# Kernel optimization log

Hardware: AMD Instinct MI355X
Metric: run time of the kernel (lower is better)

The kernel has to match this reference:

```python
import jax, jax.numpy as jnp
import numpy as np

L_PAIRS = 2
K_NEG = 64
TEMP = 0.1
EPS = 1e-8  # torch F.cosine_similarity default eps


def _cos(a, b):
    # cosine similarity along last axis, torch-style eps clamping of norms
    na = jnp.maximum(jnp.linalg.norm(a, axis=-1), EPS)
    nb = jnp.maximum(jnp.linalg.norm(b, axis=-1), EPS)
    return jnp.sum(a * b, axis=-1) / (na * nb)


def setup_inputs() -> dict:
    D, N, d = 64, 4096, 512
    key = jax.random.key(0)
    k0, k1, k2, k3 = jax.random.split(key, 4)
    return {
        "I_embeddings": jax.random.normal(k0, (D, N, d), dtype=jnp.float32),
        "g0": jax.random.normal(k1, (d,), dtype=jnp.float32),
        "g1": jax.random.normal(k2, (d,), dtype=jnp.float32),
        "g2": jax.random.normal(k3, (d,), dtype=jnp.float32),
    }


def reference(I_embeddings, g0, g1, g2):
    D, N, d = I_embeddings.shape
    T = TEMP

    # per-embedding full sum: [D, d]
    sums = jnp.sum(I_embeddings, axis=1)

    # hard-negative sums: drop the top-K rows by L2 norm per embedding
    norms = jnp.linalg.norm(I_embeddings, axis=2)              # [D, N]
    _, topk_idx = jax.lax.top_k(norms, K_NEG)                  # [D, K]
    keep = jnp.ones((D, N), dtype=bool)
    keep = keep.at[jnp.arange(D)[:, None], topk_idx].set(False)
    sums_neg = jnp.sum(I_embeddings * keep[:, :, None], axis=1)  # [D, d]

    samples = jnp.concatenate([sums, sums_neg], axis=0)        # [2D, d]

    # positive pairs (i, i+L)
    P = D - L_PAIRS
    i_idx = jnp.arange(P)
    j_idx = i_idx + L_PAIRS

    # candidates per pair: arange(2D) with i and j removed (i < j)
    base = jnp.arange(2 * D - 2)                               # [2D-2]
    cand = base[None, :] + (base[None, :] >= i_idx[:, None]).astype(base.dtype)
    cand = cand + (cand >= j_idx[:, None]).astype(cand.dtype)  # [P, 2D-2]

    # random choice of K_NEG negatives per pair (deterministic key)
    key = jax.random.key(42)
    keys = jax.random.split(key, P)
    perm = jax.vmap(lambda k: jax.random.permutation(k, 2 * D - 2))(keys)[:, :K_NEG]
    sel = jnp.take_along_axis(cand, perm, axis=1)              # [P, K]
    negs = samples[sel]                                        # [P, K, d]

    pos_ij = _cos(g1, jax.lax.stop_gradient(g2)) / T           # scalar
    pos_ji = _cos(g2, jax.lax.stop_gradient(g1)) / T           # scalar

    s_i = sums[i_idx]                                          # [P, d]
    s_j = sums[j_idx]
    sim_i = _cos(s_i[:, None, :], negs) / T                    # [P, K]
    sim_j = _cos(s_j[:, None, :], negs) / T

    # -log( exp(pos) / (exp(pos) + sum exp(sim)) ) = logaddexp(pos, lse(sim)) - pos
    loss_i = jnp.logaddexp(pos_ij, jax.nn.logsumexp(sim_i, axis=1)) - pos_ij  # [P]
    loss_j = jnp.logaddexp(pos_ji, jax.nn.logsumexp(sim_j, axis=1)) - pos_ji

    return jnp.sum(loss_i + loss_j)
```

## Files before the change

### kernel.cpp

```cpp
#include <hip/hip_runtime.h>
#include <stdint.h>

#define D_EMB   64
#define N_ROWS  4096
#define DIM     512
#define KNEG    64
#define P_PAIRS 62
#define BPE     16
#define RPB     (N_ROWS / BPE)
#define NCHUNK  (D_EMB * BPE)
#define EPSN    1e-8f
#define INV_T   10.0f
#define NEGINF  (-1e30f)

typedef float f32x4 __attribute__((ext_vector_type(4)));

__device__ __forceinline__ uint32_t rotl32(uint32_t v, uint32_t r) {
  return (v << r) | (v >> (32u - r));
}

__device__ __forceinline__ void threefry(uint32_t k0, uint32_t k1,
                                         uint32_t c0, uint32_t c1,
                                         uint32_t& o0, uint32_t& o1) {
  uint32_t ks0 = k0, ks1 = k1, ks2 = k0 ^ k1 ^ 0x1BD11BDAu;
  uint32_t x0 = c0 + ks0, x1 = c1 + ks1;
#define RG(a,b,c,d) \
  x0 += x1; x1 = rotl32(x1,a); x1 ^= x0; \
  x0 += x1; x1 = rotl32(x1,b); x1 ^= x0; \
  x0 += x1; x1 = rotl32(x1,c); x1 ^= x0; \
  x0 += x1; x1 = rotl32(x1,d); x1 ^= x0;
  RG(13,15,26,6)   x0 += ks1; x1 += ks2 + 1u;
  RG(17,29,16,24)  x0 += ks2; x1 += ks0 + 2u;
  RG(13,15,26,6)   x0 += ks0; x1 += ks1 + 3u;
  RG(17,29,16,24)  x0 += ks1; x1 += ks2 + 4u;
  RG(13,15,26,6)   x0 += ks2; x1 += ks0 + 5u;
#undef RG
  o0 = x0; o1 = x1;
}

__global__ __launch_bounds__(256, 4) void k_pass1(const float* __restrict__ I,
                                                  float* __restrict__ partial,
                                                  float* __restrict__ norms) {
  const int e = blockIdx.x >> 4, b = blockIdx.x & 15;
  const int t = threadIdx.x, lane = t & 63, w = t >> 6;
  const f32x4* base4 = reinterpret_cast<const f32x4*>(I) + (size_t)e * N_ROWS * (DIM / 4);
  const int nbase = b * RPB;
  const int wrow = w * (RPB / 4);
  __shared__ float lds[4 * DIM];
  __shared__ float nlds[RPB];
  float acc[8] = {0.f,0.f,0.f,0.f,0.f,0.f,0.f,0.f};

#define NTL(p) __builtin_nontemporal_load(p)
  for (int i = 0; i < 8; ++i) {
    const int lr = wrow + i * 8;
    const int idx = (nbase + lr) * (DIM / 4) + lane;
    f32x4 A0 = NTL(base4 + idx + 0*128), B0 = NTL(base4 + idx + 0*128 + 64);
    f32x4 A1 = NTL(base4 + idx + 1*128), B1 = NTL(base4 + idx + 1*128 + 64);
    f32x4 A2 = NTL(base4 + idx + 2*128), B2 = NTL(base4 + idx + 2*128 + 64);
    f32x4 A3 = NTL(base4 + idx + 3*128), B3 = NTL(base4 + idx + 3*128 + 64);
    f32x4 A4 = NTL(base4 + idx + 4*128), B4 = NTL(base4 + idx + 4*128 + 64);
    f32x4 A5 = NTL(base4 + idx + 5*128), B5 = NTL(base4 + idx + 5*128 + 64);
    f32x4 A6 = NTL(base4 + idx + 6*128), B6 = NTL(base4 + idx + 6*128 + 64);
    f32x4 A7 = NTL(base4 + idx + 7*128), B7 = NTL(base4 + idx + 7*128 + 64);
#undef NTL

    acc[0] += A0.x + A1.x + A2.x + A3.x + A4.x + A5.x + A6.x + A7.x;
    acc[1] += A0.y + A1.y + A2.y + A3.y + A4.y + A5.y + A6.y + A7.y;
    acc[2] += A0.z + A1.z + A2.z + A3.z + A4.z + A5.z + A6.z + A7.z;
    acc[3] += A0.w + A1.w + A2.w + A3.w + A4.w + A5.w + A6.w + A7.w;
    acc[4] += B0.x + B1.x + B2.x + B3.x + B4.x + B5.x + B6.x + B7.x;
    acc[5] += B0.y + B1.y + B2.y + B3.y + B4.y + B5.y + B6.y + B7.y;
    acc[6] += B0.z + B1.z + B2.z + B3.z + B4.z + B5.z + B6.z + B7.z;
    acc[7] += B0.w + B1.w + B2.w + B3.w + B4.w + B5.w + B6.w + B7.w;

#define SQ(r) (A##r.x*A##r.x + A##r.y*A##r.y + A##r.z*A##r.z + A##r.w*A##r.w \
             + B##r.x*B##r.x + B##r.y*B##r.y + B##r.z*B##r.z + B##r.w*B##r.w)
    float s0 = SQ(0), s1 = SQ(1), s2 = SQ(2), s3 = SQ(3);
    float s4 = SQ(4), s5 = SQ(5), s6 = SQ(6), s7 = SQ(7);
#undef SQ
#pragma unroll
    for (int off = 32; off; off >>= 1) {
      s0 += __shfl_xor(s0, off); s1 += __shfl_xor(s1, off);
      s2 += __shfl_xor(s2, off); s3 += __shfl_xor(s3, off);
      s4 += __shfl_xor(s4, off); s5 += __shfl_xor(s5, off);
      s6 += __shfl_xor(s6, off); s7 += __shfl_xor(s7, off);
    }
    if (lane == 0) {
      nlds[lr]     = sqrtf(s0); nlds[lr + 1] = sqrtf(s1);
      nlds[lr + 2] = sqrtf(s2); nlds[lr + 3] = sqrtf(s3);
      nlds[lr + 4] = sqrtf(s4); nlds[lr + 5] = sqrtf(s5);
      nlds[lr + 6] = sqrtf(s6); nlds[lr + 7] = sqrtf(s7);
    }
  }

  const int p0 = 4 * lane;
#pragma unroll
  for (int q = 0; q < 4; ++q) {
    lds[w * DIM + p0 + q]       = acc[q];
    lds[w * DIM + 256 + p0 + q] = acc[4 + q];
  }
  __syncthreads();
  float s0 = lds[t] + lds[DIM + t] + lds[2*DIM + t] + lds[3*DIM + t];
  float s1 = lds[256 + t] + lds[DIM + 256 + t] + lds[2*DIM + 256 + t] + lds[3*DIM + 256 + t];
  float* po = partial + (size_t)blockIdx.x * DIM;
  po[t] = s0;
  po[256 + t] = s1;
  norms[e * N_ROWS + nbase + t] = nlds[t];
}

#define CE(i, j) \
  { bool sw = (v##i < v##j) || (v##i == v##j && d##i > d##j);          \
    float tv = sw ? v##j : v##i; float uv = sw ? v##i : v##j;          \
    int   td = sw ? d##j : d##i; int   ud = sw ? d##i : d##j;          \
    v##i = tv; v##j = uv; d##i = td; d##j = ud; }

__global__ __launch_bounds__(512) void k_embed(const float* __restrict__ I,
                                               const float* __restrict__ partial,
                                               const float* __restrict__ norms,
                                               const float* __restrict__ g1,
                                               const float* __restrict__ g2,
                                               float* __restrict__ samples,
                                               float* __restrict__ snorm,
                                               float* __restrict__ posp,
                                               int* __restrict__ cnt2) {
  const int e = blockIdx.x;
  const int t = threadIdx.x, lane = t & 63, w = t >> 6;
  __shared__ float rA[8], rB[8], rC[8];

  if (e == D_EMB) {
    if (t == 0) cnt2[0] = 0;
    float x = g1[t], y = g2[t];
    float d = x * y, sa = x * x, sb = y * y;
#pragma unroll
    for (int off = 32; off; off >>= 1) {
      d  += __shfl_xor(d, off);
      sa += __shfl_xor(sa, off);
      sb += __shfl_xor(sb, off);
    }
    if (lane == 0) { rA[w] = d; rB[w] = sa; rC[w] = sb; }
    __syncthreads();
    if (t == 0) {
      float dt = 0.f, s1 = 0.f, s2 = 0.f;
      for (int q = 0; q < 8; ++q) { dt += rA[q]; s1 += rB[q]; s2 += rC[q]; }
      posp[0] = dt / (fmaxf(sqrtf(s1), EPSN) * fmaxf(sqrtf(s2), EPSN)) * INV_T;
    }
    return;
  }

  __shared__ float cval[8 * KNEG];
  __shared__ int   cidx[8 * KNEG];
  __shared__ int   topidx[KNEG];

  float v0 = norms[e*N_ROWS + 0*512 + t], v1 = norms[e*N_ROWS + 1*512 + t];
  float v2 = norms[e*N_ROWS + 2*512 + t], v3 = norms[e*N_ROWS + 3*512 + t];
  float v4 = norms[e*N_ROWS + 4*512 + t], v5 = norms[e*N_ROWS + 5*512 + t];
  float v6 = norms[e*N_ROWS + 6*512 + t], v7 = norms[e*N_ROWS + 7*512 + t];
  int d0 = 0*512+t, d1 = 1*512+t, d2 = 2*512+t, d3 = 3*512+t;
  int d4 = 4*512+t, d5 = 5*512+t, d6 = 6*512+t, d7 = 7*512+t;
  CE(0,1) CE(2,3) CE(4,5) CE(6,7)
  CE(0,2) CE(1,3) CE(4,6) CE(5,7)
  CE(1,2) CE(5,6)
  CE(0,4) CE(1,5) CE(2,6) CE(3,7)
  CE(2,4) CE(3,5)
  CE(1,2) CE(3,4) CE(5,6)

  for (int k = 0; k < KNEG; ++k) {
    float bv = v0; int bi = d0;
#pragma unroll
    for (int off = 32; off; off >>= 1) {
      float ov = __shfl_xor(bv, off);
      int   oi = __shfl_xor(bi, off);
      if (ov > bv || (ov == bv && oi < bi)) { bv = ov; bi = oi; }
    }
    if (lane == 0) { cval[w * KNEG + k] = bv; cidx[w * KNEG + k] = bi; }
    if (v0 == bv && d0 == bi) {
      v0=v1; d0=d1; v1=v2; d1=d2; v2=v3; d2=d3; v3=v4; d3=d4;
      v4=v5; d4=d5; v5=v6; d5=d6; v6=v7; d6=d7; v7=NEGINF; d7=0x7fffffff;
    }
  }
  __syncthreads();

  if (w == 0) {
    int p = 0;
    float hv = (lane < 8) ? cval[lane * KNEG] : NEGINF;
    int   hi = (lane < 8) ? cidx[lane * KNEG] : 0x7fffffff;
    for (int k = 0; k < KNEG; ++k) {
      float bv = hv; int bi = hi;
#pragma unroll
      for (int off = 4; off; off >>= 1) {
        float ov = __shfl_xor(bv, off, 8);
        int   oi = __shfl_xor(bi, off, 8);
        if (ov > bv || (ov == bv && oi < bi)) { bv = ov; bi = oi; }
      }
      if (lane == 0) topidx[k] = bi;
      if (lane < 8 && hv == bv && hi == bi) {
        ++p;
        hv = (p < KNEG) ? cval[lane * KNEG + p] : NEGINF;
        hi = (p < KNEG) ? cidx[lane * KNEG + p] : 0x7fffffff;
      }
    }
  }
  __syncthreads();

  float s = 0.f;
  for (int b2 = 0; b2 < BPE; ++b2)
    s += partial[(size_t)(e * BPE + b2) * DIM + t];

  const float* base = I + (size_t)e * N_ROWS * DIM;
  float a = 0.f;
#pragma unroll 4
  for (int k = 0; k < KNEG; ++k)
    a += base[(size_t)topidx[k] * DIM + t];
  float sn = s - a;

  float q1 = s * s, q2 = sn * sn;
#pragma unroll
  for (int off = 32; off; off >>= 1) {
    q1 += __shfl_xor(q1, off);
    q2 += __shfl_xor(q2, off);
  }
  if (lane == 0) { rA[w] = q1; rB[w] = q2; }
  __syncthreads();
  if (t == 0) {
    float n1 = 0.f, n2 = 0.f;
    for (int q = 0; q < 8; ++q) { n1 += rA[q]; n2 += rB[q]; }
    snorm[e]         = fmaxf(sqrtf(n1), EPSN);
    snorm[D_EMB + e] = fmaxf(sqrtf(n2), EPSN);
  }
  samples[(size_t)e * DIM + t]           = s;
  samples[(size_t)(D_EMB + e) * DIM + t] = sn;
}

__global__ __launch_bounds__(256) void k_p3p4(const float* __restrict__ samples,
                                              const float* __restrict__ snorm,
                                              const float* __restrict__ posp,
                                              float* __restrict__ pairloss,
                                              int* __restrict__ cnt2,
                                              float* __restrict__ out) {
  const int p = blockIdx.x;
  const int t = threadIdx.x, lane = t & 63, w = t >> 6;
  __shared__ uint32_t bits[126];
  __shared__ uint32_t sk[2];
  __shared__ int      sel[KNEG];
  __shared__ float    simi[KNEG], simj[KNEG];
  __shared__ int      flag;

  if (t == 0) {
    uint32_t kh, kl, a, b;
    threefry(0u, 42u, 0u, (uint32_t)p, kh, kl);
    threefry(kh, kl, 0u, 1u, a, b);
    sk[0] = a; sk[1] = b;
  }
  __syncthreads();
  if (t < 126) {
    uint32_t a, b;
    threefry(sk[0], sk[1], 0u, (uint32_t)t, a, b);
    bits[t] = a ^ b;
  }
  __syncthreads();
  if (t < 126) {
    const uint32_t myb = bits[t];
    int rank = 0;
    for (int j = 0; j < 126; ++j) {
      const uint32_t bj = bits[j];
      rank += ((bj < myb) || (bj == myb && j < t)) ? 1 : 0;
    }
    if (rank < KNEG) {
      int vv = t + (t >= p ? 1 : 0);
      vv += (vv >= p + 2 ? 1 : 0);
      sel[rank] = vv;
    }
  }
  __syncthreads();

  const float4* S = reinterpret_cast<const float4*>(samples);
  const float4 siA = S[p * 128 + lane],       siB = S[p * 128 + 64 + lane];
  const float4 sjA = S[(p + 2) * 128 + lane], sjB = S[(p + 2) * 128 + 64 + lane];
  const float ni = snorm[p], nj = snorm[p + 2];
  for (int k = w; k < KNEG; k += 4) {
    const int r = sel[k];
    const float4 vA = S[r * 128 + lane], vB = S[r * 128 + 64 + lane];
    float di = siA.x*vA.x + siA.y*vA.y + siA.z*vA.z + siA.w*vA.w
             + siB.x*vB.x + siB.y*vB.y + siB.z*vB.z + siB.w*vB.w;
    float dj = sjA.x*vA.x + sjA.y*vA.y + sjA.z*vA.z + sjA.w*vA.w
             + sjB.x*vB.x + sjB.y*vB.y + sjB.z*vB.z + sjB.w*vB.w;
#pragma unroll
    for (int off = 32; off; off >>= 1) {
      di += __shfl_xor(di, off);
      dj += __shfl_xor(dj, off);
    }
    if (lane == 0) {
      const float nr = snorm[r];
      simi[k] = di / (ni * nr) * INV_T;
      simj[k] = dj / (nj * nr) * INV_T;
    }
  }
  __syncthreads();
  if (t < KNEG) {
    const float xi = simi[t], xj = simj[t];
    float mi = xi, mj = xj;
#pragma unroll
    for (int off = 32; off; off >>= 1) {
      mi = fmaxf(mi, __shfl_xor(mi, off));
      mj = fmaxf(mj, __shfl_xor(mj, off));
    }
    float ei = expf(xi - mi), ej = expf(xj - mj);
#pragma unroll
    for (int off = 32; off; off >>= 1) {
      ei += __shfl_xor(ei, off);
      ej += __shfl_xor(ej, off);
    }
    if (t == 0) {
      const float pos = posp[0];
      const float lsei = mi + logf(ei), lsej = mj + logf(ej);
      const float li = fmaxf(pos, lsei) + log1pf(expf(-fabsf(pos - lsei))) - pos;
      const float lj = fmaxf(pos, lsej) + log1pf(expf(-fabsf(pos - lsej))) - pos;
      pairloss[p] = li + lj;
    }
  }
  __syncthreads();

  if (t == 0) {
    int old = __hip_atomic_fetch_add(cnt2, 1, __ATOMIC_ACQ_REL,
                                     __HIP_MEMORY_SCOPE_AGENT);
    flag = (old == P_PAIRS - 1) ? 1 : 0;
  }
  __syncthreads();
  const int trig = flag;
  __syncthreads();
  if (!trig) return;
  __builtin_amdgcn_fence(__ATOMIC_ACQUIRE, "agent");
  if (t < 64) {
    float vv = (t < P_PAIRS) ? pairloss[t] : 0.f;
#pragma unroll
    for (int off = 32; off; off >>= 1) vv += __shfl_xor(vv, off);
    if (t == 0) out[0] = vv;
  }
}

extern "C" void kernel_launch(void* const* d_in, const int* in_sizes, int n_in,
                              void* d_out, int out_size, void* d_ws, size_t ws_size,
                              hipStream_t stream) {
  const float* I  = (const float*)d_in[0];
  const float* g1 = (const float*)d_in[2];
  const float* g2 = (const float*)d_in[3];
  float* out = (float*)d_out;

  float* ws = (float*)d_ws;
  float* norms    = ws;
  float* partial  = ws + 262144;
  float* samples  = partial + 524288;
  float* snorm    = samples + 65536;
  float* posp     = snorm + 128;
  float* pairloss = posp + 4;
  int*   cnt2     = (int*)(pairloss + 64);

  k_pass1<<<NCHUNK,    256, 0, stream>>>(I, partial, norms);
  k_embed<<<D_EMB + 1, 512, 0, stream>>>(I, partial, norms, g1, g2,
                                         samples, snorm, posp, cnt2);
  k_p3p4 <<<P_PAIRS,   256, 0, stream>>>(samples, snorm, posp, pairloss,
                                         cnt2, out);
}
```

Measured before the change: 177.2 us.

## Fuse pass1 and per-embedding top-k via last-block atomic counter

Merges the streaming sum/norm kernel with the per-embedding top-k and sample-building kernel. Each block bumps a per-embedding atomic counter, and the last of the 16 blocks for an embedding runs the top-k, the hard-negative subtraction and the sample norms, using 256 threads. This removes one kernel launch and the gap between kernels, and lets the tail work overlap with streaming for other embeddings. The top-k now keeps a 16-value per-lane buffer with rescans in place of a sorting network, and a memset is added to reset the counters. The risk is that the last-arriving blocks carry serial top-k work, while the tail runs at half the thread count and shares LDS with the streaming blocks.

```diff
diff --git a/kernel.cpp b/kernel.cpp
--- a/kernel.cpp
+++ b/kernel.cpp
@@ -38,16 +38,48 @@
   o0 = x0; o1 = x1;
 }
 
-__global__ __launch_bounds__(256, 4) void k_pass1(const float* __restrict__ I,
-                                                  float* __restrict__ partial,
-                                                  float* __restrict__ norms) {
+__global__ __launch_bounds__(256, 4) void k_p1e(const float* __restrict__ I,
+                                                const float* __restrict__ g1,
+                                                const float* __restrict__ g2,
+                                                float* __restrict__ partial,
+                                                float* __restrict__ norms,
+                                                float* __restrict__ samples,
+                                                float* __restrict__ snorm,
+                                                float* __restrict__ posp,
+                                                int* __restrict__ cnt) {
+  const int t = threadIdx.x, lane = t & 63, w = t >> 6;
+  __shared__ float lds[4 * DIM];
+  __shared__ float nlds[RPB];
+  __shared__ float rA[4], rB[4], rC[4];
+  __shared__ int   flag;
+  __shared__ float cval[4 * KNEG];
+  __shared__ int   cidx[4 * KNEG];
+  __shared__ int   topidx[KNEG];
+
+  if (blockIdx.x == NCHUNK) {
+    float x0 = g1[t], x1 = g1[256 + t], y0 = g2[t], y1 = g2[256 + t];
+    float d = x0*y0 + x1*y1, sa = x0*x0 + x1*x1, sb = y0*y0 + y1*y1;
+#pragma unroll
+    for (int off = 32; off; off >>= 1) {
+      d  += __shfl_xor(d, off);
+      sa += __shfl_xor(sa, off);
+      sb += __shfl_xor(sb, off);
+    }
+    if (lane == 0) { rA[w] = d; rB[w] = sa; rC[w] = sb; }
+    __syncthreads();
+    if (t == 0) {
+      float dt = rA[0] + rA[1] + rA[2] + rA[3];
+      float s1 = rB[0] + rB[1] + rB[2] + rB[3];
+      float s2 = rC[0] + rC[1] + rC[2] + rC[3];
+      posp[0] = dt / (fmaxf(sqrtf(s1), EPSN) * fmaxf(sqrtf(s2), EPSN)) * INV_T;
+    }
+    return;
+  }
+
   const int e = blockIdx.x >> 4, b = blockIdx.x & 15;
-  const int t = threadIdx.x, lane = t & 63, w = t >> 6;
   const f32x4* base4 = reinterpret_cast<const f32x4*>(I) + (size_t)e * N_ROWS * (DIM / 4);
   const int nbase = b * RPB;
   const int wrow = w * (RPB / 4);
-  __shared__ float lds[4 * DIM];
-  __shared__ float nlds[RPB];
   float acc[8] = {0.f,0.f,0.f,0.f,0.f,0.f,0.f,0.f};
 
 #define NTL(p) __builtin_nontemporal_load(p)
@@ -62,7 +94,6 @@
     f32x4 A5 = NTL(base4 + idx + 5*128), B5 = NTL(base4 + idx + 5*128 + 64);
     f32x4 A6 = NTL(base4 + idx + 6*128), B6 = NTL(base4 + idx + 6*128 + 64);
     f32x4 A7 = NTL(base4 + idx + 7*128), B7 = NTL(base4 + idx + 7*128 + 64);
-#undef NTL
 
     acc[0] += A0.x + A1.x + A2.x + A3.x + A4.x + A5.x + A6.x + A7.x;
     acc[1] += A0.y + A1.y + A2.y + A3.y + A4.y + A5.y + A6.y + A7.y;
@@ -100,100 +131,73 @@
     lds[w * DIM + 256 + p0 + q] = acc[4 + q];
   }
   __syncthreads();
-  float s0 = lds[t] + lds[DIM + t] + lds[2*DIM + t] + lds[3*DIM + t];
-  float s1 = lds[256 + t] + lds[DIM + 256 + t] + lds[2*DIM + 256 + t] + lds[3*DIM + 256 + t];
-  float* po = partial + (size_t)blockIdx.x * DIM;
-  po[t] = s0;
-  po[256 + t] = s1;
-  norms[e * N_ROWS + nbase + t] = nlds[t];
-}
-
-#define CE(i, j) \
-  { bool sw = (v##i < v##j) || (v##i == v##j && d##i > d##j);          \
-    float tv = sw ? v##j : v##i; float uv = sw ? v##i : v##j;          \
-    int   td = sw ? d##j : d##i; int   ud = sw ? d##i : d##j;          \
-    v##i = tv; v##j = uv; d##i = td; d##j = ud; }
-
-__global__ __launch_bounds__(512) void k_embed(const float* __restrict__ I,
-                                               const float* __restrict__ partial,
-                                               const float* __restrict__ norms,
-                                               const float* __restrict__ g1,
-                                               const float* __restrict__ g2,
-                                               float* __restrict__ samples,
-                                               float* __restrict__ snorm,
-                                               float* __restrict__ posp,
-                                               int* __restrict__ cnt2) {
-  const int e = blockIdx.x;
-  const int t = threadIdx.x, lane = t & 63, w = t >> 6;
-  __shared__ float rA[8], rB[8], rC[8];
-
-  if (e == D_EMB) {
-    if (t == 0) cnt2[0] = 0;
-    float x = g1[t], y = g2[t];
-    float d = x * y, sa = x * x, sb = y * y;
-#pragma unroll
-    for (int off = 32; off; off >>= 1) {
-      d  += __shfl_xor(d, off);
-      sa += __shfl_xor(sa, off);
-      sb += __shfl_xor(sb, off);
-    }
-    if (lane == 0) { rA[w] = d; rB[w] = sa; rC[w] = sb; }
-    __syncthreads();
-    if (t == 0) {
-      float dt = 0.f, s1 = 0.f, s2 = 0.f;
-      for (int q = 0; q < 8; ++q) { dt += rA[q]; s1 += rB[q]; s2 += rC[q]; }
-      posp[0] = dt / (fmaxf(sqrtf(s1), EPSN) * fmaxf(sqrtf(s2), EPSN)) * INV_T;
-    }
-    return;
-  }
-
-  __shared__ float cval[8 * KNEG];
-  __shared__ int   cidx[8 * KNEG];
-  __shared__ int   topidx[KNEG];
-
-  float v0 = norms[e*N_ROWS + 0*512 + t], v1 = norms[e*N_ROWS + 1*512 + t];
-  float v2 = norms[e*N_ROWS + 2*512 + t], v3 = norms[e*N_ROWS + 3*512 + t];
-  float v4 = norms[e*N_ROWS + 4*512 + t], v5 = norms[e*N_ROWS + 5*512 + t];
-  float v6 = norms[e*N_ROWS + 6*512 + t], v7 = norms[e*N_ROWS + 7*512 + t];
-  int d0 = 0*512+t, d1 = 1*512+t, d2 = 2*512+t, d3 = 3*512+t;
-  int d4 = 4*512+t, d5 = 5*512+t, d6 = 6*512+t, d7 = 7*512+t;
-  CE(0,1) CE(2,3) CE(4,5) CE(6,7)
-  CE(0,2) CE(1,3) CE(4,6) CE(5,7)
-  CE(1,2) CE(5,6)
-  CE(0,4) CE(1,5) CE(2,6) CE(3,7)
-  CE(2,4) CE(3,5)
-  CE(1,2) CE(3,4) CE(5,6)
-
-  for (int k = 0; k < KNEG; ++k) {
-    float bv = v0; int bi = d0;
-#pragma unroll
-    for (int off = 32; off; off >>= 1) {
-      float ov = __shfl_xor(bv, off);
-      int   oi = __shfl_xor(bi, off);
-      if (ov > bv || (ov == bv && oi < bi)) { bv = ov; bi = oi; }
-    }
-    if (lane == 0) { cval[w * KNEG + k] = bv; cidx[w * KNEG + k] = bi; }
-    if (v0 == bv && d0 == bi) {
-      v0=v1; d0=d1; v1=v2; d1=d2; v2=v3; d2=d3; v3=v4; d3=d4;
-      v4=v5; d4=d5; v5=v6; d5=d6; v6=v7; d6=d7; v7=NEGINF; d7=0x7fffffff;
+  {
+    float s0 = lds[t] + lds[DIM + t] + lds[2*DIM + t] + lds[3*DIM + t];
+    float s1 = lds[256 + t] + lds[DIM + 256 + t] + lds[2*DIM + 256 + t] + lds[3*DIM + 256 + t];
+    float* po = partial + (size_t)blockIdx.x * DIM;
+    po[t] = s0;
+    po[256 + t] = s1;
+    norms[e * N_ROWS + nbase + t] = nlds[t];
+  }
+
+  __syncthreads();
+  if (t == 0) {
+    int old = __hip_atomic_fetch_add(&cnt[e], 1, __ATOMIC_ACQ_REL,
+                                     __HIP_MEMORY_SCOPE_AGENT);
+    flag = (old == BPE - 1) ? 1 : 0;
+  }
+  __syncthreads();
+  const int trig = flag;
+  __syncthreads();
+  if (!trig) return;
+  __builtin_amdgcn_fence(__ATOMIC_ACQUIRE, "agent");
+
+  {
+    float v[16];
+    const int rb = e * N_ROWS + w * 1024 + lane;
+#pragma unroll
+    for (int q = 0; q < 16; ++q) v[q] = norms[rb + q * 64];
+    float lmax = v[0]; int lq = 0;
+#pragma unroll
+    for (int q = 1; q < 16; ++q)
+      if (v[q] > lmax) { lmax = v[q]; lq = q; }
+    int lidx = w * 1024 + lq * 64 + lane;
+
+    for (int k = 0; k < KNEG; ++k) {
+      float bv = lmax; int bi = lidx;
+#pragma unroll
+      for (int off = 32; off; off >>= 1) {
+        float ov = __shfl_xor(bv, off);
+        int   oi = __shfl_xor(bi, off);
+        if (ov > bv || (ov == bv && oi < bi)) { bv = ov; bi = oi; }
+      }
+      if (lane == 0) { cval[w * KNEG + k] = bv; cidx[w * KNEG + k] = bi; }
+      if (lmax == bv && lidx == bi) {
+        v[(bi & 1023) >> 6] = NEGINF;
+        lmax = v[0]; lq = 0;
+#pragma unroll
+        for (int q = 1; q < 16; ++q)
+          if (v[q] > lmax) { lmax = v[q]; lq = q; }
+        lidx = w * 1024 + lq * 64 + lane;
+      }
     }
   }
   __syncthreads();
 
   if (w == 0) {
     int p = 0;
-    float hv = (lane < 8) ? cval[lane * KNEG] : NEGINF;
-    int   hi = (lane < 8) ? cidx[lane * KNEG] : 0x7fffffff;
+    float hv = (lane < 4) ? cval[lane * KNEG] : NEGINF;
+    int   hi = (lane < 4) ? cidx[lane * KNEG] : 0x7fffffff;
     for (int k = 0; k < KNEG; ++k) {
       float bv = hv; int bi = hi;
 #pragma unroll
-      for (int off = 4; off; off >>= 1) {
-        float ov = __shfl_xor(bv, off, 8);
-        int   oi = __shfl_xor(bi, off, 8);
+      for (int off = 2; off; off >>= 1) {
+        float ov = __shfl_xor(bv, off, 4);
+        int   oi = __shfl_xor(bi, off, 4);
         if (ov > bv || (ov == bv && oi < bi)) { bv = ov; bi = oi; }
       }
       if (lane == 0) topidx[k] = bi;
-      if (lane < 8 && hv == bv && hi == bi) {
+      if (lane < 4 && hv == bv && hi == bi) {
         ++p;
         hv = (p < KNEG) ? cval[lane * KNEG + p] : NEGINF;
         hi = (p < KNEG) ? cidx[lane * KNEG + p] : 0x7fffffff;
@@ -202,18 +206,24 @@
   }
   __syncthreads();
 
-  float s = 0.f;
-  for (int b2 = 0; b2 < BPE; ++b2)
-    s += partial[(size_t)(e * BPE + b2) * DIM + t];
-
-  const float* base = I + (size_t)e * N_ROWS * DIM;
-  float a = 0.f;
+  float s0 = 0.f, s1 = 0.f;
+  for (int b2 = 0; b2 < BPE; ++b2) {
+    const float* pp = partial + (size_t)(e * BPE + b2) * DIM;
+    s0 += pp[t];
+    s1 += pp[256 + t];
+  }
+  const float* rbase = I + (size_t)e * N_ROWS * DIM;
+  float a0 = 0.f, a1 = 0.f;
 #pragma unroll 4
-  for (int k = 0; k < KNEG; ++k)
-    a += base[(size_t)topidx[k] * DIM + t];
-  float sn = s - a;
-
-  float q1 = s * s, q2 = sn * sn;
+  for (int k = 0; k < KNEG; ++k) {
+    const float* r = rbase + (size_t)topidx[k] * DIM;
+    a0 += NTL(r + t);
+    a1 += NTL(r + 256 + t);
+  }
+#undef NTL
+  float sn0 = s0 - a0, sn1 = s1 - a1;
+
+  float q1 = s0 * s0 + s1 * s1, q2 = sn0 * sn0 + sn1 * sn1;
 #pragma unroll
   for (int off = 32; off; off >>= 1) {
     q1 += __shfl_xor(q1, off);
@@ -222,13 +232,15 @@
   if (lane == 0) { rA[w] = q1; rB[w] = q2; }
   __syncthreads();
   if (t == 0) {
-    float n1 = 0.f, n2 = 0.f;
-    for (int q = 0; q < 8; ++q) { n1 += rA[q]; n2 += rB[q]; }
+    float n1 = rA[0] + rA[1] + rA[2] + rA[3];
+    float n2 = rB[0] + rB[1] + rB[2] + rB[3];
     snorm[e]         = fmaxf(sqrtf(n1), EPSN);
     snorm[D_EMB + e] = fmaxf(sqrtf(n2), EPSN);
   }
-  samples[(size_t)e * DIM + t]           = s;
-  samples[(size_t)(D_EMB + e) * DIM + t] = sn;
+  samples[(size_t)e * DIM + t]                 = s0;
+  samples[(size_t)e * DIM + 256 + t]           = s1;
+  samples[(size_t)(D_EMB + e) * DIM + t]       = sn0;
+  samples[(size_t)(D_EMB + e) * DIM + 256 + t] = sn1;
 }
 
 __global__ __launch_bounds__(256) void k_p3p4(const float* __restrict__ samples,
@@ -353,11 +365,13 @@
   float* snorm    = samples + 65536;
   float* posp     = snorm + 128;
   float* pairloss = posp + 4;
-  int*   cnt2     = (int*)(pairloss + 64);
-
-  k_pass1<<<NCHUNK,    256, 0, stream>>>(I, partial, norms);
-  k_embed<<<D_EMB + 1, 512, 0, stream>>>(I, partial, norms, g1, g2,
-                                         samples, snorm, posp, cnt2);
-  k_p3p4 <<<P_PAIRS,   256, 0, stream>>>(samples, snorm, posp, pairloss,
+  int*   cnt      = (int*)(pairloss + 64);
+  int*   cnt2     = cnt + 64;
+
+  hipMemsetAsync(cnt, 0, 65 * sizeof(int), stream);
+
+  k_p1e <<<NCHUNK + 1, 256, 0, stream>>>(I, g1, g2, partial, norms,
+                                         samples, snorm, posp, cnt);
+  k_p3p4<<<P_PAIRS,    256, 0, stream>>>(samples, snorm, posp, pairloss,
                                          cnt2, out);
 }
```

Result: slower. 252.5 us (+42.5%).
